# Kernel tuning notes

Hardware: AMD Instinct MI355X
Metric: run time of the kernel (lower is better)

Reference implementation:

```python
import jax, jax.numpy as jnp
import numpy as np

BETA = 0.25

def setup_inputs() -> dict:
    key = jax.random.key(0)
    k1, k2, k3, k4 = jax.random.split(key, 4)
    B, C, H, W = 8, 4, 64, 64
    K = 8192
    return {
        'z_e_in': jax.random.normal(k1, (B, C, H, W), dtype=jnp.float32),
        'pq_w': jax.random.normal(k2, (C, C), dtype=jnp.float32) * 0.5,
        'pq_b': jax.random.normal(k3, (C,), dtype=jnp.float32) * 0.1,
        'codebook': jax.random.normal(k4, (K, C), dtype=jnp.float32),
    }

def reference(z_e_in, pq_w, pq_b, codebook):
    # pre_quant_conv: 1x1 conv == channel-mixing matmul
    z_e = jnp.einsum('bchw,oc->bohw', z_e_in, pq_w) + pq_b[None, :, None, None]
    B, C, H, W = z_e.shape
    z = z_e.transpose(0, 2, 3, 1).reshape(B, H * W, C)  # [B, HW, C]
    # squared Euclidean distances (argmin is invariant to sqrt in torch.cdist)
    d2 = (jnp.sum(z * z, axis=-1, keepdims=True)
          - 2.0 * jnp.einsum('bnc,kc->bnk', z, codebook)
          + jnp.sum(codebook * codebook, axis=-1))  # [B, HW, K]
    idx = jnp.argmin(d2, axis=-1)                    # [B, HW]
    z_q = codebook[idx]                               # gather, [B, HW, C]
    z_flat = z.reshape(-1, C)
    zq_flat = z_q.reshape(-1, C)
    sg = jax.lax.stop_gradient
    commitment_loss = jnp.mean((sg(zq_flat) - z_flat) ** 2)
    codebook_loss = jnp.mean((zq_flat - sg(z_flat)) ** 2)
    q_loss = codebook_loss + BETA * commitment_loss
    # straight-through estimator
    zq_st = z_flat + sg(zq_flat - z_flat)
    latent = zq_st.reshape(B, H, W, C).transpose(0, 3, 1, 2)  # [B, C, H, W]
    return latent, q_loss
```

## Files before the change

kernel.cpp:

```cpp
#include <hip/hip_runtime.h>
#include <math.h>

#define N_POINTS 32768
#define KCODES   8192
#define HW       4096
#define CHW      16384
#define NSEG     64
#define SEGLEN   (KCODES / NSEG)
#define PPT      8
#define PTILE    (256 * PPT)

#define WS_CB2    0
#define WS_CBN    131072
#define WS_PACKED 163840

__device__ __forceinline__ void compute_z(
    const float* __restrict__ ze, const float* __restrict__ w,
    const float* __restrict__ bias, int n, float zo[4], float& zz) {
  int b = n >> 12, hw = n & 4095;
  const float* p = ze + b * CHW + hw;
  float x0 = p[0], x1 = p[HW], x2 = p[2 * HW], x3 = p[3 * HW];
#pragma unroll
  for (int o = 0; o < 4; ++o) {
    float acc = __fmul_rn(x0, w[o * 4 + 0]);
    acc = __fadd_rn(acc, __fmul_rn(x1, w[o * 4 + 1]));
    acc = __fadd_rn(acc, __fmul_rn(x2, w[o * 4 + 2]));
    acc = __fadd_rn(acc, __fmul_rn(x3, w[o * 4 + 3]));
    zo[o] = __fadd_rn(acc, bias[o]);
  }
  float s = __fmul_rn(zo[0], zo[0]);
  s = __fadd_rn(s, __fmul_rn(zo[1], zo[1]));
  s = __fadd_rn(s, __fmul_rn(zo[2], zo[2]));
  s = __fadd_rn(s, __fmul_rn(zo[3], zo[3]));
  zz = s;
}

__global__ __launch_bounds__(256) void vq_init(
    const float* __restrict__ cb, float4* __restrict__ cb2,
    float* __restrict__ cbn, unsigned long long* __restrict__ packed,
    float* __restrict__ out) {
  int t = blockIdx.x * 256 + threadIdx.x;
  packed[t] = 0xFFFFFFFFFFFFFFFFull;
  if (t < KCODES) {
    float c0 = cb[t * 4 + 0], c1 = cb[t * 4 + 1];
    float c2 = cb[t * 4 + 2], c3 = cb[t * 4 + 3];
    cb2[t] = make_float4(2.f * c0, 2.f * c1, 2.f * c2, 2.f * c3);
    float s = __fmul_rn(c0, c0);
    s = __fadd_rn(s, __fmul_rn(c1, c1));
    s = __fadd_rn(s, __fmul_rn(c2, c2));
    s = __fadd_rn(s, __fmul_rn(c3, c3));
    cbn[t] = s;
  }
  if (t == 0) out[N_POINTS * 4] = 0.f;
}

__global__ __launch_bounds__(256, 3) void vq_scan(
    const float* __restrict__ ze, const float* __restrict__ w,
    const float* __restrict__ bias, const float4* __restrict__ cb2,
    const float* __restrict__ cbn, unsigned long long* __restrict__ packed) {
  __shared__ float4 s_c[SEGLEN];
  __shared__ float  s_n[SEGLEN];
  int tid = threadIdx.x;
  int k0 = blockIdx.y * SEGLEN;
  ((float*)s_c)[tid]       = ((const float*)(cb2 + k0))[tid];
  ((float*)s_c)[tid + 256] = ((const float*)(cb2 + k0))[tid + 256];
  if (tid < SEGLEN) s_n[tid] = cbn[k0 + tid];
  int n0 = blockIdx.x * PTILE + tid;
  float z[PPT][4], zz[PPT], best[PPT];
  int bidx[PPT];
#pragma unroll
  for (int p = 0; p < PPT; ++p) {
    compute_z(ze, w, bias, n0 + 256 * p, z[p], zz[p]);
    best[p] = INFINITY;
    bidx[p] = 0;
  }
  __syncthreads();
  float4 cA[4], nA;
  cA[0] = s_c[0]; cA[1] = s_c[1]; cA[2] = s_c[2]; cA[3] = s_c[3];
  nA = *(const float4*)&s_n[0];
  for (int kc = 0; kc < SEGLEN; kc += 4) {
    int kn = (kc + 4) & (SEGLEN - 1);
    float4 cB[4], nB;
    cB[0] = s_c[kn + 0]; cB[1] = s_c[kn + 1];
    cB[2] = s_c[kn + 2]; cB[3] = s_c[kn + 3];
    nB = *(const float4*)&s_n[kn];
    float cnr[4] = {nA.x, nA.y, nA.z, nA.w};
#pragma unroll
    for (int r = 0; r < 4; ++r) {
      int kk = k0 + kc + r;
#pragma unroll
      for (int p = 0; p < PPT; ++p) {
        float d = __fmul_rn(z[p][0], cA[r].x);
        d = __fadd_rn(d, __fmul_rn(z[p][1], cA[r].y));
        d = __fadd_rn(d, __fmul_rn(z[p][2], cA[r].z));
        d = __fadd_rn(d, __fmul_rn(z[p][3], cA[r].w));
        float s = __fadd_rn(__fsub_rn(zz[p], d), cnr[r]);
        if (s < best[p]) { best[p] = s; bidx[p] = kk; }
      }
    }
    cA[0] = cB[0]; cA[1] = cB[1]; cA[2] = cB[2]; cA[3] = cB[3];
    nA = nB;
  }
#pragma unroll
  for (int p = 0; p < PPT; ++p) {
    unsigned int u = __float_as_uint(best[p]);
    unsigned int so = (u & 0x80000000u) ? ~u : (u | 0x80000000u);
    unsigned long long key =
        ((unsigned long long)so << 32) | (unsigned int)bidx[p];
    atomicMin(&packed[n0 + 256 * p], key);
  }
}

__global__ __launch_bounds__(256) void vq_finish(
    const float* __restrict__ ze, const float* __restrict__ w,
    const float* __restrict__ bias, const float* __restrict__ cb,
    const unsigned long long* __restrict__ packed, float* __restrict__ out) {
  int n = blockIdx.x * 256 + threadIdx.x;
  int bidx = (unsigned int)(packed[n] & 0xFFFFFFFFull);
  float4 c = ((const float4*)cb)[bidx];
  int b = n >> 12, hw = n & 4095;
  float* o = out + b * CHW + hw;
  o[0] = c.x; o[HW] = c.y; o[2 * HW] = c.z; o[3 * HW] = c.w;
  float z[4], zz;
  compute_z(ze, w, bias, n, z, zz);
  float d0 = c.x - z[0], d1 = c.y - z[1], d2 = c.z - z[2], d3 = c.w - z[3];
  float e = d0 * d0 + d1 * d1 + d2 * d2 + d3 * d3;
#pragma unroll
  for (int off = 32; off > 0; off >>= 1) e += __shfl_down(e, off, 64);
  __shared__ float sred[4];
  if ((threadIdx.x & 63) == 0) sred[threadIdx.x >> 6] = e;
  __syncthreads();
  if (threadIdx.x == 0) {
    float t = (sred[0] + sred[1]) + (sred[2] + sred[3]);
    atomicAdd(out + (N_POINTS * 4), t * (1.25f / 131072.f));
  }
}

extern "C" void kernel_launch(void* const* d_in, const int* in_sizes, int n_in,
                              void* d_out, int out_size, void* d_ws, size_t ws_size,
                              hipStream_t stream) {
  const float* ze   = (const float*)d_in[0];
  const float* w    = (const float*)d_in[1];
  const float* bias = (const float*)d_in[2];
  const float* cb   = (const float*)d_in[3];

  char* ws = (char*)d_ws;
  float4* cb2 = (float4*)(ws + WS_CB2);
  float*  cbn = (float*)(ws + WS_CBN);
  unsigned long long* packed = (unsigned long long*)(ws + WS_PACKED);
  float* out = (float*)d_out;

  vq_init<<<128, 256, 0, stream>>>(cb, cb2, cbn, packed, out);
  vq_scan<<<dim3(N_POINTS / PTILE, NSEG), 256, 0, stream>>>(
      ze, w, bias, cb2, cbn, packed);
  vq_finish<<<128, 256, 0, stream>>>(ze, w, bias, cb, packed, out);
}
```

Before: 116.0 us.

## Pack point pairs into float2 for packed FP32 math and fold codebook prep into scan

The distance loop now holds two points per 2-wide float vector, so the compiler can emit packed FP32 multiply/add instructions (v_pk_mul/v_pk_add) on MI355X. Contraction is turned off to keep rounding identical to the reference. The separate init kernel is removed: each scan block scales its own codebook segment by two and computes the code norms while loading it into shared memory, and the workspace and loss initialisation become memset calls. This trades one kernel launch and a global round trip for a small amount of redundant per-block prep, and the argmin compare/select still runs as scalar code.

```diff
diff --git a/kernel.cpp b/kernel.cpp
--- a/kernel.cpp
+++ b/kernel.cpp
@@ -8,11 +8,12 @@
 #define NSEG     64
 #define SEGLEN   (KCODES / NSEG)
 #define PPT      8
+#define QPT      (PPT / 2)
 #define PTILE    (256 * PPT)
 
-#define WS_CB2    0
-#define WS_CBN    131072
-#define WS_PACKED 163840
+#define WS_PACKED 0
+
+typedef float v2f __attribute__((ext_vector_type(2)));
 
 __device__ __forceinline__ void compute_z(
     const float* __restrict__ ze, const float* __restrict__ w,
@@ -35,44 +36,38 @@
   zz = s;
 }
 
-__global__ __launch_bounds__(256) void vq_init(
-    const float* __restrict__ cb, float4* __restrict__ cb2,
-    float* __restrict__ cbn, unsigned long long* __restrict__ packed,
-    float* __restrict__ out) {
-  int t = blockIdx.x * 256 + threadIdx.x;
-  packed[t] = 0xFFFFFFFFFFFFFFFFull;
-  if (t < KCODES) {
-    float c0 = cb[t * 4 + 0], c1 = cb[t * 4 + 1];
-    float c2 = cb[t * 4 + 2], c3 = cb[t * 4 + 3];
-    cb2[t] = make_float4(2.f * c0, 2.f * c1, 2.f * c2, 2.f * c3);
-    float s = __fmul_rn(c0, c0);
-    s = __fadd_rn(s, __fmul_rn(c1, c1));
-    s = __fadd_rn(s, __fmul_rn(c2, c2));
-    s = __fadd_rn(s, __fmul_rn(c3, c3));
-    cbn[t] = s;
-  }
-  if (t == 0) out[N_POINTS * 4] = 0.f;
-}
-
 __global__ __launch_bounds__(256, 3) void vq_scan(
     const float* __restrict__ ze, const float* __restrict__ w,
-    const float* __restrict__ bias, const float4* __restrict__ cb2,
-    const float* __restrict__ cbn, unsigned long long* __restrict__ packed) {
+    const float* __restrict__ bias, const float* __restrict__ cb,
+    unsigned long long* __restrict__ packed) {
+#pragma clang fp contract(off)
   __shared__ float4 s_c[SEGLEN];
   __shared__ float  s_n[SEGLEN];
   int tid = threadIdx.x;
   int k0 = blockIdx.y * SEGLEN;
-  ((float*)s_c)[tid]       = ((const float*)(cb2 + k0))[tid];
-  ((float*)s_c)[tid + 256] = ((const float*)(cb2 + k0))[tid + 256];
-  if (tid < SEGLEN) s_n[tid] = cbn[k0 + tid];
+  if (tid < SEGLEN) {
+    float4 cv = ((const float4*)cb)[k0 + tid];
+    s_c[tid] = make_float4(2.f * cv.x, 2.f * cv.y, 2.f * cv.z, 2.f * cv.w);
+    float s = __fmul_rn(cv.x, cv.x);
+    s = __fadd_rn(s, __fmul_rn(cv.y, cv.y));
+    s = __fadd_rn(s, __fmul_rn(cv.z, cv.z));
+    s = __fadd_rn(s, __fmul_rn(cv.w, cv.w));
+    s_n[tid] = s;
+  }
   int n0 = blockIdx.x * PTILE + tid;
-  float z[PPT][4], zz[PPT], best[PPT];
+  v2f zp[4][QPT], zz2[QPT];
+  float best[PPT];
   int bidx[PPT];
 #pragma unroll
-  for (int p = 0; p < PPT; ++p) {
-    compute_z(ze, w, bias, n0 + 256 * p, z[p], zz[p]);
-    best[p] = INFINITY;
-    bidx[p] = 0;
+  for (int q = 0; q < QPT; ++q) {
+    float za[4], zb[4], zza, zzb;
+    compute_z(ze, w, bias, n0 + 256 * (2 * q + 0), za, zza);
+    compute_z(ze, w, bias, n0 + 256 * (2 * q + 1), zb, zzb);
+#pragma unroll
+    for (int c = 0; c < 4; ++c) zp[c][q] = (v2f){za[c], zb[c]};
+    zz2[q] = (v2f){zza, zzb};
+    best[2 * q] = INFINITY; best[2 * q + 1] = INFINITY;
+    bidx[2 * q] = 0; bidx[2 * q + 1] = 0;
   }
   __syncthreads();
   float4 cA[4], nA;
@@ -89,13 +84,14 @@
     for (int r = 0; r < 4; ++r) {
       int kk = k0 + kc + r;
 #pragma unroll
-      for (int p = 0; p < PPT; ++p) {
-        float d = __fmul_rn(z[p][0], cA[r].x);
-        d = __fadd_rn(d, __fmul_rn(z[p][1], cA[r].y));
-        d = __fadd_rn(d, __fmul_rn(z[p][2], cA[r].z));
-        d = __fadd_rn(d, __fmul_rn(z[p][3], cA[r].w));
-        float s = __fadd_rn(__fsub_rn(zz[p], d), cnr[r]);
-        if (s < best[p]) { best[p] = s; bidx[p] = kk; }
+      for (int q = 0; q < QPT; ++q) {
+        v2f d = zp[0][q] * cA[r].x;
+        d = d + zp[1][q] * cA[r].y;
+        d = d + zp[2][q] * cA[r].z;
+        d = d + zp[3][q] * cA[r].w;
+        v2f s = (zz2[q] - d) + cnr[r];
+        if (s.x < best[2 * q])     { best[2 * q] = s.x;     bidx[2 * q] = kk; }
+        if (s.y < best[2 * q + 1]) { best[2 * q + 1] = s.y; bidx[2 * q + 1] = kk; }
       }
     }
     cA[0] = cB[0]; cA[1] = cB[1]; cA[2] = cB[2]; cA[3] = cB[3];
@@ -144,14 +140,13 @@
   const float* bias = (const float*)d_in[2];
   const float* cb   = (const float*)d_in[3];
 
-  char* ws = (char*)d_ws;
-  float4* cb2 = (float4*)(ws + WS_CB2);
-  float*  cbn = (float*)(ws + WS_CBN);
-  unsigned long long* packed = (unsigned long long*)(ws + WS_PACKED);
+  unsigned long long* packed = (unsigned long long*)((char*)d_ws + WS_PACKED);
   float* out = (float*)d_out;
 
-  vq_init<<<128, 256, 0, stream>>>(cb, cb2, cbn, packed, out);
+  hipMemsetAsync(packed, 0xFF, (size_t)N_POINTS * 8, stream);
+  hipMemsetAsync(out + (N_POINTS * 4), 0, sizeof(float), stream);
+
   vq_scan<<<dim3(N_POINTS / PTILE, NSEG), 256, 0, stream>>>(
-      ze, w, bias, cb2, cbn, packed);
+      ze, w, bias, cb, packed);
   vq_finish<<<128, 256, 0, stream>>>(ze, w, bias, cb, packed, out);
 }
```

Result: slower. 131.2 us (+13.0%).
